# Kernel optimization log

Measured on AMD Instinct MI355X. Metric: run time of the kernel, lower is better.

Reference implementation:

```python
import jax, jax.numpy as jnp
import numpy as np

N_NODES = 100000
N_EDGES = 640000
D = 128
EPS = 1e-5

def _full_layer_norm(x):
    # torch layer_norm with normalized_shape == x.shape: stats over ALL elements
    mu = jnp.mean(x)
    var = jnp.mean(jnp.square(x - mu))  # biased variance
    return (x - mu) * jax.lax.rsqrt(var + EPS)

def setup_inputs() -> dict:
    key = jax.random.key(0)
    k1, k2, k3, k4, k5 = jax.random.split(key, 5)
    scale1 = 1.0 / np.sqrt(D)
    scale2 = 1.0 / np.sqrt(2 * D)
    return {
        "edge_features": jax.random.normal(k1, (N_EDGES, D), dtype=jnp.float32),
        "node_features": jax.random.normal(k2, (N_NODES, D), dtype=jnp.float32),
        "edge_indices": jax.random.randint(k3, (N_EDGES, 2), 0, N_NODES, dtype=jnp.int32),
        "W1": jax.random.normal(k4, (D, D), dtype=jnp.float32) * scale1,
        "b1": jnp.zeros((D,), dtype=jnp.float32),
        "W2": jax.random.normal(k5, (2 * D, D), dtype=jnp.float32) * scale2,
        "b2": jnp.zeros((D,), dtype=jnp.float32),
    }

def reference(edge_features, node_features, edge_indices, W1, b1, W2, b2):
    # node MLP: linear -> whole-tensor layernorm -> gelu
    h = node_features @ W1 + b1                       # [N, D]
    h = jax.nn.gelu(_full_layer_norm(h), approximate=False)
    # gather source-node features onto edges
    src = edge_indices[:, 0]
    dst = edge_indices[:, 1]
    gathered = h[src]                                 # [E, D]
    e = jnp.concatenate([edge_features, gathered], axis=1)  # [E, 2D]
    e = e @ W2 + b2                                   # [E, D]
    e = jax.nn.gelu(_full_layer_norm(e), approximate=False)
    # scatter-mean (include_self=False): nodes with no in-edges stay 0
    seg_sum = jax.ops.segment_sum(e, dst, num_segments=N_NODES)       # [N, D]
    counts = jax.ops.segment_sum(jnp.ones((e.shape[0],), e.dtype), dst,
                                 num_segments=N_NODES)                 # [N]
    counts = counts[:, None]
    return jnp.where(counts > 0, seg_sum / jnp.maximum(counts, 1.0), 0.0)
```

## Files before the change

kernel.cpp:

```cpp
#include <hip/hip_runtime.h>
#include <hip/hip_bf16.h>
#include <math.h>

typedef __bf16 bf16;
typedef bf16 bf16x8 __attribute__((ext_vector_type(8)));
typedef float f32x4 __attribute__((ext_vector_type(4)));
typedef unsigned short ushort_t;
typedef unsigned long long u64;

#define N_NODES 100000
#define N_EDGES 640000
#define DD 128
#define MAXDEG 64
#define STAT_SCALE 1048576.0

__device__ __forceinline__ float gelu_fast(float x) {
    float z2 = x * (1.595769122f + 0.071354816f * x * x);
    return x * __builtin_amdgcn_rcpf(1.0f + __expf(-z2));
}

__device__ __forceinline__ ushort_t bf16_bits(float x) {
    bf16 h = (bf16)x;
    return __builtin_bit_cast(ushort_t, h);
}

__device__ __forceinline__ float bits_to_f(ushort_t u) {
    return __uint_as_float(((unsigned)u) << 16);
}

__device__ __forceinline__ long long to_fixed(double x) {
    return (long long)(x * STAT_SCALE + (x >= 0.0 ? 0.5 : -0.5));
}

__device__ __forceinline__ void stats_atomic(float lsum, float lsq, float* red,
                                             u64* dsum, u64* dsq) {
    int tid = threadIdx.x;
    red[tid] = lsum; __syncthreads();
    for (int s = 128; s > 0; s >>= 1) { if (tid < s) red[tid] += red[tid + s]; __syncthreads(); }
    float bs = red[0]; __syncthreads();
    red[tid] = lsq; __syncthreads();
    for (int s = 128; s > 0; s >>= 1) { if (tid < s) red[tid] += red[tid + s]; __syncthreads(); }
    if (tid == 0) {
        atomicAdd(dsum, (u64)to_fixed((double)bs));
        atomicAdd(dsq,  (u64)to_fixed((double)red[0]));
    }
}

__device__ __forceinline__ void stats_decode(const u64* stats, double cnt,
                                             float* mu, float* rs) {
    long long ss = (long long)stats[0], sq = (long long)stats[1];
    double mu_d = ((double)ss / STAT_SCALE) / cnt;
    double var  = ((double)sq / STAT_SCALE) / cnt - mu_d * mu_d;
    *mu = (float)mu_d;
    *rs = (float)(1.0 / sqrt(var + 1e-5));
}

#define PACK8(dstp, a, b) { \
    ushort_t o_[8] = {bf16_bits(a.x), bf16_bits(a.y), bf16_bits(a.z), bf16_bits(a.w), \
                      bf16_bits(b.x), bf16_bits(b.y), bf16_bits(b.z), bf16_bits(b.w)}; \
    *(uint4*)(dstp) = *(const uint4*)o_; }

#define K1_TILES 1563
__global__ __launch_bounds__(256) void k1_gemm1(
    const float* __restrict__ nf, const float* __restrict__ W1,
    const float* __restrict__ b1, ushort_t* __restrict__ hpre,
    u64* __restrict__ stats, int nblocks)
{
    __shared__ bf16 Ash[64 * 136];
    __shared__ float red[256];
    const int tid = threadIdx.x;
    const int lane = tid & 63;
    const int w = tid >> 6;
    const int l15 = lane & 15, l4 = lane >> 4;

    bf16x8 bfrag[4][2];
    #pragma unroll
    for (int s = 0; s < 4; ++s)
        #pragma unroll
        for (int t = 0; t < 2; ++t) {
            int n = w * 32 + t * 16 + l15;
            #pragma unroll
            for (int j = 0; j < 8; ++j)
                bfrag[s][t][j] = (bf16)W1[(s * 32 + l4 * 8 + j) * DD + n];
        }
    float4 bias4[2];
    bias4[0] = *(const float4*)&b1[w * 32 + l4 * 4];
    bias4[1] = *(const float4*)&b1[w * 32 + 16 + l4 * 4];

    float lsum = 0.f, lsq = 0.f;
    const int srow = tid >> 2;
    const int q = tid & 3;

    float4 efr[8];
    {
        int grow = min(blockIdx.x * 64 + srow, N_NODES - 1);
        const float4* p = (const float4*)&nf[(size_t)grow * DD + q * 32];
        #pragma unroll
        for (int u = 0; u < 8; ++u) efr[u] = p[u];
    }

    for (int tile = blockIdx.x; tile < K1_TILES; tile += nblocks) {
        const int rbase = tile * 64;
        __syncthreads();
        #pragma unroll
        for (int u = 0; u < 4; ++u)
            PACK8(&Ash[srow * 136 + q * 32 + u * 8], efr[2 * u], efr[2 * u + 1]);
        __syncthreads();
        int nt = tile + nblocks;
        if (nt < K1_TILES) {
            int grow = min(nt * 64 + srow, N_NODES - 1);
            const float4* p = (const float4*)&nf[(size_t)grow * DD + q * 32];
            #pragma unroll
            for (int u = 0; u < 8; ++u) efr[u] = p[u];
        }
        f32x4 acc[4][2];
        #pragma unroll
        for (int r = 0; r < 4; ++r)
            #pragma unroll
            for (int t = 0; t < 2; ++t)
                acc[r][t] = (f32x4){0.f, 0.f, 0.f, 0.f};
        #pragma unroll
        for (int s = 0; s < 4; ++s)
            #pragma unroll
            for (int r = 0; r < 4; ++r) {
                bf16x8 a = *(const bf16x8*)&Ash[(r * 16 + l15) * 136 + s * 32 + l4 * 8];
                acc[r][0] = __builtin_amdgcn_mfma_f32_16x16x32_bf16(bfrag[s][0], a, acc[r][0], 0, 0, 0);
                acc[r][1] = __builtin_amdgcn_mfma_f32_16x16x32_bf16(bfrag[s][1], a, acc[r][1], 0, 0, 0);
            }
        #pragma unroll
        for (int r = 0; r < 4; ++r) {
            int row = rbase + r * 16 + l15;
            if (row < N_NODES) {
                #pragma unroll
                for (int t = 0; t < 2; ++t) {
                    int col = w * 32 + t * 16 + l4 * 4;
                    ushort_t o[4];
                    #pragma unroll
                    for (int j = 0; j < 4; ++j) {
                        float v = acc[r][t][j] + bias4[t][j];
                        lsum += v; lsq += v * v;
                        o[j] = bf16_bits(v);
                    }
                    *(uint2*)&hpre[(size_t)row * DD + col] = *(const uint2*)o;
                }
            }
        }
    }
    stats_atomic(lsum, lsq, red, &stats[0], &stats[1]);
}

__global__ __launch_bounds__(256) void k2b_gemmh(
    const ushort_t* __restrict__ hpre, const float* __restrict__ W2,
    const u64* __restrict__ stats, ushort_t* __restrict__ hh, int nblocks)
{
    __shared__ bf16 Ash[64 * 136];
    float mu, rs;
    stats_decode(stats, (double)N_NODES * DD, &mu, &rs);

    const int tid = threadIdx.x;
    const int lane = tid & 63;
    const int w = tid >> 6;
    const int l15 = lane & 15, l4 = lane >> 4;

    bf16x8 bfrag[4][2];
    #pragma unroll
    for (int s = 0; s < 4; ++s)
        #pragma unroll
        for (int t = 0; t < 2; ++t) {
            int n = w * 32 + t * 16 + l15;
            #pragma unroll
            for (int j = 0; j < 8; ++j)
                bfrag[s][t][j] = (bf16)W2[(DD + s * 32 + l4 * 8 + j) * DD + n];
        }

    const int srow = tid >> 2;
    const int q = tid & 3;

    uint4 hr[4];
    {
        int grow = min(blockIdx.x * 64 + srow, N_NODES - 1);
        const uint4* p = (const uint4*)&hpre[(size_t)grow * DD + q * 32];
        #pragma unroll
        for (int u = 0; u < 4; ++u) hr[u] = p[u];
    }

    for (int tile = blockIdx.x; tile < K1_TILES; tile += nblocks) {
        const int rbase = tile * 64;
        __syncthreads();
        #pragma unroll
        for (int u = 0; u < 4; ++u) {
            const ushort_t* in = (const ushort_t*)&hr[u];
            ushort_t o[8];
            #pragma unroll
            for (int j = 0; j < 8; ++j)
                o[j] = bf16_bits(gelu_fast((bits_to_f(in[j]) - mu) * rs));
            *(uint4*)&Ash[srow * 136 + q * 32 + u * 8] = *(const uint4*)o;
        }
        __syncthreads();
        int nt = tile + nblocks;
        if (nt < K1_TILES) {
            int grow = min(nt * 64 + srow, N_NODES - 1);
            const uint4* p = (const uint4*)&hpre[(size_t)grow * DD + q * 32];
            #pragma unroll
            for (int u = 0; u < 4; ++u) hr[u] = p[u];
        }
        f32x4 acc[4][2];
        #pragma unroll
        for (int r = 0; r < 4; ++r)
            #pragma unroll
            for (int t = 0; t < 2; ++t)
                acc[r][t] = (f32x4){0.f, 0.f, 0.f, 0.f};
        #pragma unroll
        for (int s = 0; s < 4; ++s)
            #pragma unroll
            for (int r = 0; r < 4; ++r) {
                bf16x8 a = *(const bf16x8*)&Ash[(r * 16 + l15) * 136 + s * 32 + l4 * 8];
                acc[r][0] = __builtin_amdgcn_mfma_f32_16x16x32_bf16(bfrag[s][0], a, acc[r][0], 0, 0, 0);
                acc[r][1] = __builtin_amdgcn_mfma_f32_16x16x32_bf16(bfrag[s][1], a, acc[r][1], 0, 0, 0);
            }
        #pragma unroll
        for (int r = 0; r < 4; ++r) {
            int row = rbase + r * 16 + l15;
            if (row < N_NODES) {
                #pragma unroll
                for (int t = 0; t < 2; ++t) {
                    int col = w * 32 + t * 16 + l4 * 4;
                    ushort_t o[4];
                    #pragma unroll
                    for (int j = 0; j < 4; ++j)
                        o[j] = bf16_bits(acc[r][t][j]);
                    *(uint2*)&hh[(size_t)row * DD + col] = *(const uint2*)o;
                }
            }
        }
    }
}

#define K4_TILES (N_EDGES / 64)
__global__ __launch_bounds__(256) void k4_gemm2(
    const float* __restrict__ ef, const ushort_t* __restrict__ hh,
    const int* __restrict__ eidx, const float* __restrict__ W2,
    const float* __restrict__ b2, ushort_t* __restrict__ e0,
    u64* __restrict__ stats, int nblocks)
{
    __shared__ bf16 Ash[64 * 136];
    __shared__ float red[256];
    const int tid = threadIdx.x;
    const int lane = tid & 63;
    const int w = tid >> 6;
    const int l15 = lane & 15, l4 = lane >> 4;

    bf16x8 bfrag[4][2];
    #pragma unroll
    for (int s = 0; s < 4; ++s)
        #pragma unroll
        for (int t = 0; t < 2; ++t) {
            int n = w * 32 + t * 16 + l15;
            #pragma unroll
            for (int j = 0; j < 8; ++j)
                bfrag[s][t][j] = (bf16)W2[(s * 32 + l4 * 8 + j) * DD + n];
        }
    float4 bias4[2];
    bias4[0] = *(const float4*)&b2[w * 32 + l4 * 4];
    bias4[1] = *(const float4*)&b2[w * 32 + 16 + l4 * 4];

    float lsum = 0.f, lsq = 0.f;
    const int srow = tid >> 2;
    const int q = tid & 3;

    float4 efr[8];
    {
        const float4* p = (const float4*)&ef[(size_t)(blockIdx.x * 64 + srow) * DD + q * 32];
        #pragma unroll
        for (int u = 0; u < 8; ++u) efr[u] = p[u];
    }

    for (int tile = blockIdx.x; tile < K4_TILES; tile += nblocks) {
        const int ebase = tile * 64;
        int srcv[4];
        #pragma unroll
        for (int r = 0; r < 4; ++r)
            srcv[r] = eidx[(size_t)(ebase + r * 16 + l15) * 2];
        uint2 hv[4][2];
        #pragma unroll
        for (int r = 0; r < 4; ++r)
            #pragma unroll
            for (int t = 0; t < 2; ++t)
                hv[r][t] = *(const uint2*)&hh[(size_t)srcv[r] * DD + w * 32 + t * 16 + l4 * 4];
        __syncthreads();
        #pragma unroll
        for (int u = 0; u < 4; ++u)
            PACK8(&Ash[srow * 136 + q * 32 + u * 8], efr[2 * u], efr[2 * u + 1]);
        __syncthreads();
        int nt = tile + nblocks;
        if (nt < K4_TILES) {
            const float4* p = (const float4*)&ef[(size_t)(nt * 64 + srow) * DD + q * 32];
            #pragma unroll
            for (int u = 0; u < 8; ++u) efr[u] = p[u];
        }
        f32x4 acc[4][2];
        #pragma unroll
        for (int r = 0; r < 4; ++r)
            #pragma unroll
            for (int t = 0; t < 2; ++t)
                acc[r][t] = (f32x4){0.f, 0.f, 0.f, 0.f};
        #pragma unroll
        for (int s = 0; s < 4; ++s)
            #pragma unroll
            for (int r = 0; r < 4; ++r) {
                bf16x8 a = *(const bf16x8*)&Ash[(r * 16 + l15) * 136 + s * 32 + l4 * 8];
                acc[r][0] = __builtin_amdgcn_mfma_f32_16x16x32_bf16(bfrag[s][0], a, acc[r][0], 0, 0, 0);
                acc[r][1] = __builtin_amdgcn_mfma_f32_16x16x32_bf16(bfrag[s][1], a, acc[r][1], 0, 0, 0);
            }
        #pragma unroll
        for (int r = 0; r < 4; ++r) {
            int row = ebase + r * 16 + l15;
            #pragma unroll
            for (int t = 0; t < 2; ++t) {
                int col = w * 32 + t * 16 + l4 * 4;
                float hadd[4] = {bits_to_f((ushort_t)(hv[r][t].x & 0xffff)),
                                 bits_to_f((ushort_t)(hv[r][t].x >> 16)),
                                 bits_to_f((ushort_t)(hv[r][t].y & 0xffff)),
                                 bits_to_f((ushort_t)(hv[r][t].y >> 16))};
                ushort_t o[4];
                #pragma unroll
                for (int j = 0; j < 4; ++j) {
                    float v = acc[r][t][j] + bias4[t][j] + hadd[j];
                    lsum += v; lsq += v * v;
                    o[j] = bf16_bits(v);
                }
                *(uint2*)&e0[(size_t)row * DD + col] = *(const uint2*)o;
            }
        }
    }
    stats_atomic(lsum, lsq, red, &stats[2], &stats[3]);
}

__global__ __launch_bounds__(256) void k7_fill(
    const int* __restrict__ eidx, int* __restrict__ cnt, int* __restrict__ slot)
{
    int e = blockIdx.x * 256 + threadIdx.x;
    if (e >= N_EDGES) return;
    int dst = eidx[(size_t)e * 2 + 1];
    int pos = atomicAdd(&cnt[dst], 1);
    if (pos < MAXDEG) slot[dst * MAXDEG + pos] = e;
}

__global__ __launch_bounds__(256) void k8_gather(
    const ushort_t* __restrict__ e0v, const int* __restrict__ slot,
    const int* __restrict__ cnt, const u64* __restrict__ stats,
    float* __restrict__ out)
{
    float mu, rs;
    stats_decode(stats + 2, (double)N_EDGES * DD, &mu, &rs);
    int node = (int)((blockIdx.x * 256 + threadIdx.x) >> 6);
    int lane = threadIdx.x & 63;
    if (node >= N_NODES) return;
    int c = cnt[node];
    int m = min(c, MAXDEG);
    int myslot = (lane < m) ? slot[node * MAXDEG + lane] : 0;
    float a0 = 0.f, a1 = 0.f;
    const size_t off = (size_t)(lane * 2);
    int j = 0;
    for (; j + 4 <= m; j += 4) {
        int ea = __shfl(myslot, j);
        int eb = __shfl(myslot, j + 1);
        int ec = __shfl(myslot, j + 2);
        int ed = __shfl(myslot, j + 3);
        unsigned ua = *(const unsigned*)&e0v[(size_t)ea * DD + off];
        unsigned ub = *(const unsigned*)&e0v[(size_t)eb * DD + off];
        unsigned uc = *(const unsigned*)&e0v[(size_t)ec * DD + off];
        unsigned ud = *(const unsigned*)&e0v[(size_t)ed * DD + off];
        a0 += gelu_fast((__uint_as_float(ua << 16) - mu) * rs);
        a1 += gelu_fast((__uint_as_float(ua & 0xffff0000u) - mu) * rs);
        a0 += gelu_fast((__uint_as_float(ub << 16) - mu) * rs);
        a1 += gelu_fast((__uint_as_float(ub & 0xffff0000u) - mu) * rs);
        a0 += gelu_fast((__uint_as_float(uc << 16) - mu) * rs);
        a1 += gelu_fast((__uint_as_float(uc & 0xffff0000u) - mu) * rs);
        a0 += gelu_fast((__uint_as_float(ud << 16) - mu) * rs);
        a1 += gelu_fast((__uint_as_float(ud & 0xffff0000u) - mu) * rs);
    }
    for (; j < m; ++j) {
        int ea = __shfl(myslot, j);
        unsigned ua = *(const unsigned*)&e0v[(size_t)ea * DD + off];
        a0 += gelu_fast((__uint_as_float(ua << 16) - mu) * rs);
        a1 += gelu_fast((__uint_as_float(ua & 0xffff0000u) - mu) * rs);
    }
    float inv = c > 0 ? 1.0f / (float)c : 0.f;
    float2 res = {a0 * inv, a1 * inv};
    *(float2*)&out[(size_t)node * DD + lane * 2] = res;
}

extern "C" void kernel_launch(void* const* d_in, const int* in_sizes, int n_in,
                              void* d_out, int out_size, void* d_ws, size_t ws_size,
                              hipStream_t stream) {
    const float* ef  = (const float*)d_in[0];
    const float* nf  = (const float*)d_in[1];
    const int*   eix = (const int*)d_in[2];
    const float* W1  = (const float*)d_in[3];
    const float* b1  = (const float*)d_in[4];
    const float* W2  = (const float*)d_in[5];
    const float* b2  = (const float*)d_in[6];
    float* out = (float*)d_out;
    char* ws = (char*)d_ws;

    ushort_t* hpre  = (ushort_t*)(ws + 0);
    ushort_t* hh    = (ushort_t*)(ws + 25600000);
    ushort_t* e0    = (ushort_t*)(ws + 51200000);
    int*      cnt   = (int*)(ws + 215040000);
    u64*      stats = (u64*)(ws + 215440000);
    int*      slot  = (int*)(ws + 215440064);

    hipMemsetAsync(cnt, 0, 400064, stream);
    k1_gemm1<<<521, 256, 0, stream>>>(nf, W1, b1, hpre, stats, 521);
    k2b_gemmh<<<521, 256, 0, stream>>>(hpre, W2, stats, hh, 521);
    k7_fill<<<2500, 256, 0, stream>>>(eix, cnt, slot);
    k4_gemm2<<<1250, 256, 0, stream>>>(ef, hh, eix, W2, b2, e0, stats, 1250);
    k8_gather<<<25000, 256, 0, stream>>>(e0, slot, cnt, stats, out);
}
```

Measured before the change: 302.0 us.

## Split gather wave into half-waves over edges, replace memset with init kernel, retune grids

```diff
diff --git a/kernel.cpp b/kernel.cpp
--- a/kernel.cpp
+++ b/kernel.cpp
@@ -59,6 +59,14 @@
     ushort_t o_[8] = {bf16_bits(a.x), bf16_bits(a.y), bf16_bits(a.z), bf16_bits(a.w), \
                       bf16_bits(b.x), bf16_bits(b.y), bf16_bits(b.z), bf16_bits(b.w)}; \
     *(uint4*)(dstp) = *(const uint4*)o_; }
+
+__global__ __launch_bounds__(256) void k0_init(int* __restrict__ cnt,
+                                               u64* __restrict__ stats)
+{
+    int i = blockIdx.x * 256 + threadIdx.x;
+    if (i < N_NODES) cnt[i] = 0;
+    if (i < 4) stats[i] = 0ull;
+}
 
 #define K1_TILES 1563
 __global__ __launch_bounds__(256) void k1_gemm1(
@@ -356,39 +364,56 @@
     int node = (int)((blockIdx.x * 256 + threadIdx.x) >> 6);
     int lane = threadIdx.x & 63;
     if (node >= N_NODES) return;
+    const int hl = lane >> 5;
+    const int l31 = lane & 31;
     int c = cnt[node];
     int m = min(c, MAXDEG);
     int myslot = (lane < m) ? slot[node * MAXDEG + lane] : 0;
-    float a0 = 0.f, a1 = 0.f;
-    const size_t off = (size_t)(lane * 2);
-    int j = 0;
-    for (; j + 4 <= m; j += 4) {
-        int ea = __shfl(myslot, j);
-        int eb = __shfl(myslot, j + 1);
-        int ec = __shfl(myslot, j + 2);
-        int ed = __shfl(myslot, j + 3);
-        unsigned ua = *(const unsigned*)&e0v[(size_t)ea * DD + off];
-        unsigned ub = *(const unsigned*)&e0v[(size_t)eb * DD + off];
-        unsigned uc = *(const unsigned*)&e0v[(size_t)ec * DD + off];
-        unsigned ud = *(const unsigned*)&e0v[(size_t)ed * DD + off];
-        a0 += gelu_fast((__uint_as_float(ua << 16) - mu) * rs);
-        a1 += gelu_fast((__uint_as_float(ua & 0xffff0000u) - mu) * rs);
-        a0 += gelu_fast((__uint_as_float(ub << 16) - mu) * rs);
-        a1 += gelu_fast((__uint_as_float(ub & 0xffff0000u) - mu) * rs);
-        a0 += gelu_fast((__uint_as_float(uc << 16) - mu) * rs);
-        a1 += gelu_fast((__uint_as_float(uc & 0xffff0000u) - mu) * rs);
-        a0 += gelu_fast((__uint_as_float(ud << 16) - mu) * rs);
-        a1 += gelu_fast((__uint_as_float(ud & 0xffff0000u) - mu) * rs);
-    }
-    for (; j < m; ++j) {
-        int ea = __shfl(myslot, j);
-        unsigned ua = *(const unsigned*)&e0v[(size_t)ea * DD + off];
-        a0 += gelu_fast((__uint_as_float(ua << 16) - mu) * rs);
-        a1 += gelu_fast((__uint_as_float(ua & 0xffff0000u) - mu) * rs);
-    }
-    float inv = c > 0 ? 1.0f / (float)c : 0.f;
-    float2 res = {a0 * inv, a1 * inv};
-    *(float2*)&out[(size_t)node * DD + lane * 2] = res;
+    float a0 = 0.f, a1 = 0.f, a2 = 0.f, a3 = 0.f;
+    const size_t off = (size_t)(l31 * 4);
+
+    int steps = m >> 1;
+    int s = 0;
+    for (; s + 2 <= steps; s += 2) {
+        int eA = __shfl(myslot, 2 * s + hl);
+        int eB = __shfl(myslot, 2 * (s + 1) + hl);
+        uint2 uA = *(const uint2*)&e0v[(size_t)eA * DD + off];
+        uint2 uB = *(const uint2*)&e0v[(size_t)eB * DD + off];
+        a0 += gelu_fast((__uint_as_float(uA.x << 16) - mu) * rs);
+        a1 += gelu_fast((__uint_as_float(uA.x & 0xffff0000u) - mu) * rs);
+        a2 += gelu_fast((__uint_as_float(uA.y << 16) - mu) * rs);
+        a3 += gelu_fast((__uint_as_float(uA.y & 0xffff0000u) - mu) * rs);
+        a0 += gelu_fast((__uint_as_float(uB.x << 16) - mu) * rs);
+        a1 += gelu_fast((__uint_as_float(uB.x & 0xffff0000u) - mu) * rs);
+        a2 += gelu_fast((__uint_as_float(uB.y << 16) - mu) * rs);
+        a3 += gelu_fast((__uint_as_float(uB.y & 0xffff0000u) - mu) * rs);
+    }
+    for (; s < steps; ++s) {
+        int eA = __shfl(myslot, 2 * s + hl);
+        uint2 uA = *(const uint2*)&e0v[(size_t)eA * DD + off];
+        a0 += gelu_fast((__uint_as_float(uA.x << 16) - mu) * rs);
+        a1 += gelu_fast((__uint_as_float(uA.x & 0xffff0000u) - mu) * rs);
+        a2 += gelu_fast((__uint_as_float(uA.y << 16) - mu) * rs);
+        a3 += gelu_fast((__uint_as_float(uA.y & 0xffff0000u) - mu) * rs);
+    }
+    if (m & 1) {
+        int eA = __shfl(myslot, m - 1);
+        uint2 uA = *(const uint2*)&e0v[(size_t)eA * DD + off];
+        float g0 = gelu_fast((__uint_as_float(uA.x << 16) - mu) * rs);
+        float g1 = gelu_fast((__uint_as_float(uA.x & 0xffff0000u) - mu) * rs);
+        float g2 = gelu_fast((__uint_as_float(uA.y << 16) - mu) * rs);
+        float g3 = gelu_fast((__uint_as_float(uA.y & 0xffff0000u) - mu) * rs);
+        if (hl == 0) { a0 += g0; a1 += g1; a2 += g2; a3 += g3; }
+    }
+    a0 += __shfl_xor(a0, 32);
+    a1 += __shfl_xor(a1, 32);
+    a2 += __shfl_xor(a2, 32);
+    a3 += __shfl_xor(a3, 32);
+    if (hl == 0) {
+        float inv = c > 0 ? 1.0f / (float)c : 0.f;
+        float4 res = {a0 * inv, a1 * inv, a2 * inv, a3 * inv};
+        *(float4*)&out[(size_t)node * DD + l31 * 4] = res;
+    }
 }
 
 extern "C" void kernel_launch(void* const* d_in, const int* in_sizes, int n_in,
@@ -411,10 +436,10 @@
     u64*      stats = (u64*)(ws + 215440000);
     int*      slot  = (int*)(ws + 215440064);
 
-    hipMemsetAsync(cnt, 0, 400064, stream);
-    k1_gemm1<<<521, 256, 0, stream>>>(nf, W1, b1, hpre, stats, 521);
-    k2b_gemmh<<<521, 256, 0, stream>>>(hpre, W2, stats, hh, 521);
+    k0_init<<<391, 256, 0, stream>>>(cnt, stats);
+    k1_gemm1<<<782, 256, 0, stream>>>(nf, W1, b1, hpre, stats, 782);
+    k2b_gemmh<<<782, 256, 0, stream>>>(hpre, W2, stats, hh, 782);
     k7_fill<<<2500, 256, 0, stream>>>(eix, cnt, slot);
-    k4_gemm2<<<1250, 256, 0, stream>>>(ef, hh, eix, W2, b2, e0, stats, 1250);
+    k4_gemm2<<<2500, 256, 0, stream>>>(ef, hh, eix, W2, b2, e0, stats, 2500);
     k8_gather<<<25000, 256, 0, stream>>>(e0, slot, cnt, stats, out);
 }
```

Result: no change. 306.7 us (+1.5%).
